# Kernel optimization log

Hardware: AMD Instinct MI355X
Metric: run time of the kernel (lower is better)

## Reference

```python
import jax, jax.numpy as jnp
import numpy as np

C, H, W = 3, 2048, 2048
N_ANN = 64
P = 512  # patch resolution
RESIZE_FRAC = 0.5  # deterministic midpoint of resize_range=(0.25, 0.75)
MIN_SIZE = 10


def setup_inputs() -> dict:
    key = jax.random.key(0)
    k1, k2, k3, k4 = jax.random.split(key, 4)
    image = jax.random.normal(k1, (C, H, W), jnp.float32)
    patch = jax.random.uniform(k2, (C, P, P), jnp.float32)
    # build valid normalized xyxy boxes (x1<x2, y1<y2) inside the image
    centers = jax.random.uniform(k3, (N_ANN, 2), minval=0.2, maxval=0.8)
    sizes = jax.random.uniform(k4, (N_ANN, 2), minval=0.10, maxval=0.30)
    xy1 = jnp.clip(centers - sizes / 2, 0.0, 1.0)
    xy2 = jnp.clip(centers + sizes / 2, 0.0, 1.0)
    annotations = jnp.concatenate([xy1, xy2], axis=1).astype(jnp.float32)  # [N,4] xyxy
    return {"image": image, "annotations": annotations, "patch": patch}


def reference(image, annotations, patch):
    """MODE_CENTER_BBOX forward: for each bbox, bilinearly resize the patch to
    wh x wh (wh = min(bbox_w, bbox_h) * RESIZE_FRAC, >= MIN_SIZE), then paste it
    centered in the bbox (clamped to the image). embed_patch's mask arithmetic
    (image_mask*image + patch_mask*patch) is exactly a region overwrite."""
    c, h, w = image.shape
    # normalized_annotations=True: scale by [W, H, W, H] then floor to long
    ann = np.asarray(annotations * jnp.array([w, h, w, h], jnp.float32)).astype(np.int64)
    img = image
    for x1, y1, x2, y2 in ann:
        bw, bh = int(x2 - x1), int(y2 - y1)
        wh = max(int(min(bw, bh) * RESIZE_FRAC), MIN_SIZE)
        rp = jax.image.resize(patch, (c, wh, wh), method="bilinear")
        x = int(x1) + bw // 2 - wh // 2
        y = int(y1) + bh // 2 - wh // 2
        y = max(min(h - wh, y), 0)
        x = max(min(w - wh, x), 0)
        img = img.at[:, y:y + wh, x:x + wh].set(rp)
    return img
```

## Files before the change

kernel.cpp:

```cpp
#include <hip/hip_runtime.h>

#define CCH 3
#define HH 2048
#define WW 2048
#define NANN 64
#define PSZ 512
#define HWIMG (HH * WW)
#define PP (PSZ * PSZ)
#define WHMAX 308
#define OYB 4
#define CHS ((size_t)PSZ * WHMAX)

__global__ void prep_kernel(const float* __restrict__ ann, int* __restrict__ meta) {
    int a = threadIdx.x;
    if (a >= NANN) return;
    float x1f = ann[a * 4 + 0] * (float)WW;
    float y1f = ann[a * 4 + 1] * (float)HH;
    float x2f = ann[a * 4 + 2] * (float)WW;
    float y2f = ann[a * 4 + 3] * (float)HH;
    int x1 = (int)x1f, y1 = (int)y1f, x2 = (int)x2f, y2 = (int)y2f;
    int bw = x2 - x1, bh = y2 - y1;
    int mn = bw < bh ? bw : bh;
    int wh = mn / 2;
    if (wh < 10) wh = 10;
    int x = x1 + bw / 2 - wh / 2;
    int y = y1 + bh / 2 - wh / 2;
    y = min(HH - wh, y); y = max(y, 0);
    x = min(WW - wh, x); x = max(x, 0);
    meta[a * 4 + 0] = x;
    meta[a * 4 + 1] = y;
    meta[a * 4 + 2] = wh;
    meta[a * 4 + 3] = 0;
}

__global__ __launch_bounds__(256) void resize_y4_kernel(
    const float* __restrict__ patch, const int* __restrict__ meta,
    float* __restrict__ tmp)
{
    const int a   = blockIdx.y;
    const int oy0 = blockIdx.x * OYB;
    const int wh  = meta[a * 4 + 2];
    if (oy0 >= wh) return;

    const int xx = threadIdx.x * 2;
    const float inv = 512.0f / (float)wh;
    const float rs  = (float)wh / 512.0f;

    float syf[OYB];
#pragma unroll
    for (int i = 0; i < OYB; ++i)
        syf[i] = ((float)(oy0 + i) + 0.5f) * inv - 0.5f;

    const int ylast = min(oy0 + OYB - 1, wh - 1);
    const float syfL = ((float)ylast + 0.5f) * inv - 0.5f;
    const int ylo = max(0,       (int)ceilf(syf[0] - inv));
    const int yhi = min(PSZ - 1, (int)floorf(syfL + inv));

    float2 ac[OYB][3];
    float dy[OYB];
#pragma unroll
    for (int i = 0; i < OYB; ++i) {
        dy[i] = 0.f;
#pragma unroll
        for (int c = 0; c < 3; ++c) { ac[i][c].x = 0.f; ac[i][c].y = 0.f; }
    }

    const float* p = patch + xx;
#pragma unroll 2
    for (int yy = ylo; yy <= yhi; ++yy) {
        const float* row = p + yy * PSZ;
        float2 v0 = *(const float2*)(row);
        float2 v1 = *(const float2*)(row + PP);
        float2 v2 = *(const float2*)(row + 2 * PP);
#pragma unroll
        for (int i = 0; i < OYB; ++i) {
            float w = fmaxf(0.f, 1.f - fabsf(syf[i] - (float)yy) * rs);
            dy[i] += w;
            ac[i][0].x = fmaf(w, v0.x, ac[i][0].x);
            ac[i][0].y = fmaf(w, v0.y, ac[i][0].y);
            ac[i][1].x = fmaf(w, v1.x, ac[i][1].x);
            ac[i][1].y = fmaf(w, v1.y, ac[i][1].y);
            ac[i][2].x = fmaf(w, v2.x, ac[i][2].x);
            ac[i][2].y = fmaf(w, v2.y, ac[i][2].y);
        }
    }

#pragma unroll
    for (int i = 0; i < OYB; ++i) {
        int oy = oy0 + i;
        if (oy < wh) {
            float s = 1.0f / dy[i];
            float* t = tmp + ((size_t)(a * 3) * WHMAX + oy) * PSZ + xx;
            float2 o0 = { ac[i][0].x * s, ac[i][0].y * s };
            float2 o1 = { ac[i][1].x * s, ac[i][1].y * s };
            float2 o2 = { ac[i][2].x * s, ac[i][2].y * s };
            *(float2*)(t)           = o0;
            *(float2*)(t + CHS)     = o1;
            *(float2*)(t + 2 * CHS) = o2;
        }
    }
}

__global__ __launch_bounds__(256) void composite_kernel(
    const float* __restrict__ img, const float* __restrict__ tmp,
    const int* __restrict__ meta, float* __restrict__ out)
{
    __shared__ int sax[NANN], say[NANN], sawh[NANN];
    __shared__ unsigned long long smask;

    const int tid = threadIdx.x;
    const int bx = blockIdx.x * 64;
    const int by = blockIdx.y * 4;

    if (tid < NANN) {
        int x = meta[tid * 4 + 0];
        int y = meta[tid * 4 + 1];
        int wh = meta[tid * 4 + 2];
        sax[tid] = x; say[tid] = y; sawh[tid] = wh;
        bool ov = (x < bx + 64) && (x + wh > bx) && (y < by + 4) && (y + wh > by);
        unsigned long long m = __ballot(ov);
        if (tid == 0) smask = m;
    }
    __syncthreads();

    const int px = bx + (tid & 63);
    const int py = by + (tid >> 6);
    const int idx = py * WW + px;

    unsigned long long m = smask;
    int hit = -1;
    while (m) {
        int a = 63 - __clzll(m);
        if (px >= sax[a] && px < sax[a] + sawh[a] &&
            py >= say[a] && py < say[a] + sawh[a]) { hit = a; break; }
        m &= ~(1ull << a);
    }

    if (hit < 0) {
        out[idx]             = img[idx];
        out[idx + HWIMG]     = img[idx + HWIMG];
        out[idx + 2 * HWIMG] = img[idx + 2 * HWIMG];
        return;
    }

    const int wh = sawh[hit];
    const int jx = px - sax[hit];
    const int jy = py - say[hit];

    const float inv = 512.0f / (float)wh;
    const float rs  = (float)wh / 512.0f;
    const float sxf = ((float)jx + 0.5f) * inv - 0.5f;
    const int xlo = max(0,       (int)ceilf(sxf - inv));
    const int xhi = min(PSZ - 1, (int)floorf(sxf + inv));

    int kstart = xlo & ~3;
    if (kstart > 496) kstart = 496;

    const float* tb = tmp + ((size_t)(hit * 3) * WHMAX + jy) * PSZ;

    if (xhi - kstart <= 15) {
        float r0[16], r1[16], r2[16];
#pragma unroll
        for (int u = 0; u < 4; ++u) {
            float4 qa = *(const float4*)(tb + kstart + 4 * u);
            float4 qb = *(const float4*)(tb + CHS + kstart + 4 * u);
            float4 qc = *(const float4*)(tb + 2 * CHS + kstart + 4 * u);
            r0[4 * u + 0] = qa.x; r0[4 * u + 1] = qa.y; r0[4 * u + 2] = qa.z; r0[4 * u + 3] = qa.w;
            r1[4 * u + 0] = qb.x; r1[4 * u + 1] = qb.y; r1[4 * u + 2] = qb.z; r1[4 * u + 3] = qb.w;
            r2[4 * u + 0] = qc.x; r2[4 * u + 1] = qc.y; r2[4 * u + 2] = qc.z; r2[4 * u + 3] = qc.w;
        }
        float dx = 0.f, a0 = 0.f, a1 = 0.f, a2 = 0.f;
#pragma unroll
        for (int j = 0; j < 16; ++j) {
            int pos = kstart + j;
            float w = (pos <= xhi) ? fmaxf(0.f, 1.f - fabsf(sxf - (float)pos) * rs) : 0.f;
            dx += w;
            a0 = fmaf(w, r0[j], a0);
            a1 = fmaf(w, r1[j], a1);
            a2 = fmaf(w, r2[j], a2);
        }
        const float s = 1.0f / dx;
        out[idx]             = a0 * s;
        out[idx + HWIMG]     = a1 * s;
        out[idx + 2 * HWIMG] = a2 * s;
    } else {
        float dx = 0.f;
        for (int x = xlo; x <= xhi; ++x)
            dx += fmaxf(0.f, 1.f - fabsf(sxf - (float)x) * rs);
        float a0 = 0.f, a1 = 0.f, a2 = 0.f;
        for (int x = xlo; x <= xhi; ++x) {
            float w = fmaxf(0.f, 1.f - fabsf(sxf - (float)x) * rs);
            a0 = fmaf(w, tb[x],           a0);
            a1 = fmaf(w, tb[x + CHS],     a1);
            a2 = fmaf(w, tb[x + 2 * CHS], a2);
        }
        const float s = 1.0f / dx;
        out[idx]             = a0 * s;
        out[idx + HWIMG]     = a1 * s;
        out[idx + 2 * HWIMG] = a2 * s;
    }
}

extern "C" void kernel_launch(void* const* d_in, const int* in_sizes, int n_in,
                              void* d_out, int out_size, void* d_ws, size_t ws_size,
                              hipStream_t stream) {
    const float* img   = (const float*)d_in[0];
    const float* ann   = (const float*)d_in[1];
    const float* patch = (const float*)d_in[2];
    float* out = (float*)d_out;

    int*   meta = (int*)d_ws;
    float* tmp  = (float*)((char*)d_ws + 4096);

    hipLaunchKernelGGL(prep_kernel, dim3(1), dim3(64), 0, stream, ann, meta);
    hipLaunchKernelGGL(resize_y4_kernel, dim3((WHMAX + OYB - 1) / OYB, NANN), dim3(256),
                       0, stream, patch, meta, tmp);
    hipLaunchKernelGGL(composite_kernel, dim3(WW / 64, HH / 4), dim3(256), 0, stream,
                       img, tmp, meta, out);
}
```

Before: 61.01 us.

## Replace full-image composite with memcpy plus per-annotation paste kernel

The per-pixel composite kernel, which scanned annotation masks over the whole image, is replaced. The image is now copied to the output with a device-to-device memcpy, and a paste kernel then walks only each annotation's patch region. A pixel is skipped when a later annotation covers it, which keeps last-writer-wins semantics without any ordering between blocks. The aim is to stop running overlap searches over pixels that no box touches. The cost is that overlapped pixels get an O(N) later-box check, and the output region is written twice (copy, then paste).

```diff
diff --git a/kernel.cpp b/kernel.cpp
--- a/kernel.cpp
+++ b/kernel.cpp
@@ -101,51 +101,37 @@
     }
 }
 
-__global__ __launch_bounds__(256) void composite_kernel(
-    const float* __restrict__ img, const float* __restrict__ tmp,
-    const int* __restrict__ meta, float* __restrict__ out)
+__global__ __launch_bounds__(256) void paste_kernel(
+    const float* __restrict__ tmp, const int* __restrict__ meta,
+    float* __restrict__ out)
 {
     __shared__ int sax[NANN], say[NANN], sawh[NANN];
-    __shared__ unsigned long long smask;
+
+    const int a  = blockIdx.z;
+    const int wh = meta[a * 4 + 2];
+    const int jx0 = blockIdx.x * 64;
+    const int jy0 = blockIdx.y * 4;
+    if (jx0 >= wh || jy0 >= wh) return;
 
     const int tid = threadIdx.x;
-    const int bx = blockIdx.x * 64;
-    const int by = blockIdx.y * 4;
-
     if (tid < NANN) {
-        int x = meta[tid * 4 + 0];
-        int y = meta[tid * 4 + 1];
-        int wh = meta[tid * 4 + 2];
-        sax[tid] = x; say[tid] = y; sawh[tid] = wh;
-        bool ov = (x < bx + 64) && (x + wh > bx) && (y < by + 4) && (y + wh > by);
-        unsigned long long m = __ballot(ov);
-        if (tid == 0) smask = m;
+        sax[tid]  = meta[tid * 4 + 0];
+        say[tid]  = meta[tid * 4 + 1];
+        sawh[tid] = meta[tid * 4 + 2];
     }
     __syncthreads();
 
-    const int px = bx + (tid & 63);
-    const int py = by + (tid >> 6);
-    const int idx = py * WW + px;
-
-    unsigned long long m = smask;
-    int hit = -1;
-    while (m) {
-        int a = 63 - __clzll(m);
-        if (px >= sax[a] && px < sax[a] + sawh[a] &&
-            py >= say[a] && py < say[a] + sawh[a]) { hit = a; break; }
-        m &= ~(1ull << a);
-    }
-
-    if (hit < 0) {
-        out[idx]             = img[idx];
-        out[idx + HWIMG]     = img[idx + HWIMG];
-        out[idx + 2 * HWIMG] = img[idx + 2 * HWIMG];
-        return;
-    }
-
-    const int wh = sawh[hit];
-    const int jx = px - sax[hit];
-    const int jy = py - say[hit];
+    const int jx = jx0 + (tid & 63);
+    const int jy = jy0 + (tid >> 6);
+    if (jx >= wh || jy >= wh) return;
+
+    const int px = sax[a] + jx;
+    const int py = say[a] + jy;
+
+    for (int b = a + 1; b < NANN; ++b) {
+        if (px >= sax[b] && px < sax[b] + sawh[b] &&
+            py >= say[b] && py < say[b] + sawh[b]) return;
+    }
 
     const float inv = 512.0f / (float)wh;
     const float rs  = (float)wh / 512.0f;
@@ -156,7 +142,8 @@
     int kstart = xlo & ~3;
     if (kstart > 496) kstart = 496;
 
-    const float* tb = tmp + ((size_t)(hit * 3) * WHMAX + jy) * PSZ;
+    const float* tb = tmp + ((size_t)(a * 3) * WHMAX + jy) * PSZ;
+    const int idx = py * WW + px;
 
     if (xhi - kstart <= 15) {
         float r0[16], r1[16], r2[16];
@@ -215,6 +202,9 @@
     hipLaunchKernelGGL(prep_kernel, dim3(1), dim3(64), 0, stream, ann, meta);
     hipLaunchKernelGGL(resize_y4_kernel, dim3((WHMAX + OYB - 1) / OYB, NANN), dim3(256),
                        0, stream, patch, meta, tmp);
-    hipLaunchKernelGGL(composite_kernel, dim3(WW / 64, HH / 4), dim3(256), 0, stream,
-                       img, tmp, meta, out);
-}
+    hipMemcpyAsync(out, img, (size_t)out_size * sizeof(float),
+                   hipMemcpyDeviceToDevice, stream);
+    hipLaunchKernelGGL(paste_kernel,
+                       dim3((WHMAX + 63) / 64, (WHMAX + 3) / 4, NANN), dim3(256),
+                       0, stream, tmp, meta, out);
+}
```

After: 94.66 us. 55.2% more time.

## Widen composite tiles, add float4 fast path, swizzle block order, add 8-tap path

Applied to the files above, without the earlier changes.

Each composite block now covers a 256x4 tile instead of 64x4, with each thread handling four pixels. Tiles that no box overlaps take a float4 copy fast path. Block IDs are permuted with a multiplicative hash, which should spread patch-covered tiles evenly across compute units. The horizontal resample gains an 8-tap specialisation for small patches, loading only two float4s per channel. The costs are fewer blocks and more per-thread work in overlapped tiles, which may reduce latency hiding.

```diff
diff --git a/kernel.cpp b/kernel.cpp
--- a/kernel.cpp
+++ b/kernel.cpp
@@ -10,6 +10,9 @@
 #define WHMAX 308
 #define OYB 4
 #define CHS ((size_t)PSZ * WHMAX)
+#define GX (WW / 256)
+#define GY (HH / 4)
+#define NTILE (GX * GY)
 
 __global__ void prep_kernel(const float* __restrict__ ann, int* __restrict__ meta) {
     int a = threadIdx.x;
@@ -101,6 +104,81 @@
     }
 }
 
+__device__ __forceinline__ void resample_px(
+    const float* __restrict__ tmp, int a, int wh, int jx, int jy,
+    float* __restrict__ out, int idx)
+{
+    const float inv = 512.0f / (float)wh;
+    const float rs  = (float)wh / 512.0f;
+    const float sxf = ((float)jx + 0.5f) * inv - 0.5f;
+    const int xlo = max(0,       (int)ceilf(sxf - inv));
+    const int xhi = min(PSZ - 1, (int)floorf(sxf + inv));
+
+    const float* tb = tmp + ((size_t)(a * 3) * WHMAX + jy) * PSZ;
+    float dx = 0.f, a0 = 0.f, a1 = 0.f, a2 = 0.f;
+
+    const int ka = xlo & ~3;
+    const int k8 = min(ka, 504);
+
+    if (xhi - k8 <= 7) {
+        float wgt[8];
+#pragma unroll
+        for (int j = 0; j < 8; ++j) {
+            int pos = k8 + j;
+            float w = (pos <= xhi) ? fmaxf(0.f, 1.f - fabsf(sxf - (float)pos) * rs) : 0.f;
+            wgt[j] = w; dx += w;
+        }
+#pragma unroll
+        for (int u = 0; u < 2; ++u) {
+            float4 qa = *(const float4*)(tb + k8 + 4 * u);
+            float4 qb = *(const float4*)(tb + CHS + k8 + 4 * u);
+            float4 qc = *(const float4*)(tb + 2 * CHS + k8 + 4 * u);
+            a0 = fmaf(wgt[4*u+0], qa.x, a0); a0 = fmaf(wgt[4*u+1], qa.y, a0);
+            a0 = fmaf(wgt[4*u+2], qa.z, a0); a0 = fmaf(wgt[4*u+3], qa.w, a0);
+            a1 = fmaf(wgt[4*u+0], qb.x, a1); a1 = fmaf(wgt[4*u+1], qb.y, a1);
+            a1 = fmaf(wgt[4*u+2], qb.z, a1); a1 = fmaf(wgt[4*u+3], qb.w, a1);
+            a2 = fmaf(wgt[4*u+0], qc.x, a2); a2 = fmaf(wgt[4*u+1], qc.y, a2);
+            a2 = fmaf(wgt[4*u+2], qc.z, a2); a2 = fmaf(wgt[4*u+3], qc.w, a2);
+        }
+    } else {
+        const int k16 = min(ka, 496);
+        if (xhi - k16 <= 15) {
+            float wgt[16];
+#pragma unroll
+            for (int j = 0; j < 16; ++j) {
+                int pos = k16 + j;
+                float w = (pos <= xhi) ? fmaxf(0.f, 1.f - fabsf(sxf - (float)pos) * rs) : 0.f;
+                wgt[j] = w; dx += w;
+            }
+#pragma unroll
+            for (int u = 0; u < 4; ++u) {
+                float4 qa = *(const float4*)(tb + k16 + 4 * u);
+                float4 qb = *(const float4*)(tb + CHS + k16 + 4 * u);
+                float4 qc = *(const float4*)(tb + 2 * CHS + k16 + 4 * u);
+                a0 = fmaf(wgt[4*u+0], qa.x, a0); a0 = fmaf(wgt[4*u+1], qa.y, a0);
+                a0 = fmaf(wgt[4*u+2], qa.z, a0); a0 = fmaf(wgt[4*u+3], qa.w, a0);
+                a1 = fmaf(wgt[4*u+0], qb.x, a1); a1 = fmaf(wgt[4*u+1], qb.y, a1);
+                a1 = fmaf(wgt[4*u+2], qb.z, a1); a1 = fmaf(wgt[4*u+3], qb.w, a1);
+                a2 = fmaf(wgt[4*u+0], qc.x, a2); a2 = fmaf(wgt[4*u+1], qc.y, a2);
+                a2 = fmaf(wgt[4*u+2], qc.z, a2); a2 = fmaf(wgt[4*u+3], qc.w, a2);
+            }
+        } else {
+            for (int x = xlo; x <= xhi; ++x)
+                dx += fmaxf(0.f, 1.f - fabsf(sxf - (float)x) * rs);
+            for (int x = xlo; x <= xhi; ++x) {
+                float w = fmaxf(0.f, 1.f - fabsf(sxf - (float)x) * rs);
+                a0 = fmaf(w, tb[x],           a0);
+                a1 = fmaf(w, tb[x + CHS],     a1);
+                a2 = fmaf(w, tb[x + 2 * CHS], a2);
+            }
+        }
+    }
+    const float s = 1.0f / dx;
+    out[idx]             = a0 * s;
+    out[idx + HWIMG]     = a1 * s;
+    out[idx + 2 * HWIMG] = a2 * s;
+}
+
 __global__ __launch_bounds__(256) void composite_kernel(
     const float* __restrict__ img, const float* __restrict__ tmp,
     const int* __restrict__ meta, float* __restrict__ out)
@@ -109,95 +187,57 @@
     __shared__ unsigned long long smask;
 
     const int tid = threadIdx.x;
-    const int bx = blockIdx.x * 64;
-    const int by = blockIdx.y * 4;
+    const int lid = blockIdx.y * GX + blockIdx.x;
+    const int sid = (lid * 1543) & (NTILE - 1);
+    const int bx = (sid & (GX - 1)) * 256;
+    const int by = (sid / GX) * 4;
 
     if (tid < NANN) {
         int x = meta[tid * 4 + 0];
         int y = meta[tid * 4 + 1];
         int wh = meta[tid * 4 + 2];
         sax[tid] = x; say[tid] = y; sawh[tid] = wh;
-        bool ov = (x < bx + 64) && (x + wh > bx) && (y < by + 4) && (y + wh > by);
-        unsigned long long m = __ballot(ov);
-        if (tid == 0) smask = m;
+        bool ov = (x < bx + 256) && (x + wh > bx) && (y < by + 4) && (y + wh > by);
+        unsigned long long mm = __ballot(ov);
+        if (tid == 0) smask = mm;
     }
     __syncthreads();
 
-    const int px = bx + (tid & 63);
+    const unsigned long long tmask = smask;
+
+    if (tmask == 0) {
+        const int x0  = bx + (tid & 63) * 4;
+        const int py  = by + (tid >> 6);
+        const int idx = py * WW + x0;
+        *(float4*)(out + idx)             = *(const float4*)(img + idx);
+        *(float4*)(out + idx + HWIMG)     = *(const float4*)(img + idx + HWIMG);
+        *(float4*)(out + idx + 2 * HWIMG) = *(const float4*)(img + idx + 2 * HWIMG);
+        return;
+    }
+
+    const int lx = tid & 63;
     const int py = by + (tid >> 6);
-    const int idx = py * WW + px;
-
-    unsigned long long m = smask;
-    int hit = -1;
-    while (m) {
-        int a = 63 - __clzll(m);
-        if (px >= sax[a] && px < sax[a] + sawh[a] &&
-            py >= say[a] && py < say[a] + sawh[a]) { hit = a; break; }
-        m &= ~(1ull << a);
-    }
-
-    if (hit < 0) {
-        out[idx]             = img[idx];
-        out[idx + HWIMG]     = img[idx + HWIMG];
-        out[idx + 2 * HWIMG] = img[idx + 2 * HWIMG];
-        return;
-    }
-
-    const int wh = sawh[hit];
-    const int jx = px - sax[hit];
-    const int jy = py - say[hit];
-
-    const float inv = 512.0f / (float)wh;
-    const float rs  = (float)wh / 512.0f;
-    const float sxf = ((float)jx + 0.5f) * inv - 0.5f;
-    const int xlo = max(0,       (int)ceilf(sxf - inv));
-    const int xhi = min(PSZ - 1, (int)floorf(sxf + inv));
-
-    int kstart = xlo & ~3;
-    if (kstart > 496) kstart = 496;
-
-    const float* tb = tmp + ((size_t)(hit * 3) * WHMAX + jy) * PSZ;
-
-    if (xhi - kstart <= 15) {
-        float r0[16], r1[16], r2[16];
-#pragma unroll
-        for (int u = 0; u < 4; ++u) {
-            float4 qa = *(const float4*)(tb + kstart + 4 * u);
-            float4 qb = *(const float4*)(tb + CHS + kstart + 4 * u);
-            float4 qc = *(const float4*)(tb + 2 * CHS + kstart + 4 * u);
-            r0[4 * u + 0] = qa.x; r0[4 * u + 1] = qa.y; r0[4 * u + 2] = qa.z; r0[4 * u + 3] = qa.w;
-            r1[4 * u + 0] = qb.x; r1[4 * u + 1] = qb.y; r1[4 * u + 2] = qb.z; r1[4 * u + 3] = qb.w;
-            r2[4 * u + 0] = qc.x; r2[4 * u + 1] = qc.y; r2[4 * u + 2] = qc.z; r2[4 * u + 3] = qc.w;
-        }
-        float dx = 0.f, a0 = 0.f, a1 = 0.f, a2 = 0.f;
-#pragma unroll
-        for (int j = 0; j < 16; ++j) {
-            int pos = kstart + j;
-            float w = (pos <= xhi) ? fmaxf(0.f, 1.f - fabsf(sxf - (float)pos) * rs) : 0.f;
-            dx += w;
-            a0 = fmaf(w, r0[j], a0);
-            a1 = fmaf(w, r1[j], a1);
-            a2 = fmaf(w, r2[j], a2);
-        }
-        const float s = 1.0f / dx;
-        out[idx]             = a0 * s;
-        out[idx + HWIMG]     = a1 * s;
-        out[idx + 2 * HWIMG] = a2 * s;
-    } else {
-        float dx = 0.f;
-        for (int x = xlo; x <= xhi; ++x)
-            dx += fmaxf(0.f, 1.f - fabsf(sxf - (float)x) * rs);
-        float a0 = 0.f, a1 = 0.f, a2 = 0.f;
-        for (int x = xlo; x <= xhi; ++x) {
-            float w = fmaxf(0.f, 1.f - fabsf(sxf - (float)x) * rs);
-            a0 = fmaf(w, tb[x],           a0);
-            a1 = fmaf(w, tb[x + CHS],     a1);
-            a2 = fmaf(w, tb[x + 2 * CHS], a2);
-        }
-        const float s = 1.0f / dx;
-        out[idx]             = a0 * s;
-        out[idx + HWIMG]     = a1 * s;
-        out[idx + 2 * HWIMG] = a2 * s;
+#pragma unroll
+    for (int it = 0; it < 4; ++it) {
+        const int px  = bx + it * 64 + lx;
+        const int idx = py * WW + px;
+
+        unsigned long long m = tmask;
+        int hit = -1;
+        while (m) {
+            int a = 63 - __clzll(m);
+            if (px >= sax[a] && px < sax[a] + sawh[a] &&
+                py >= say[a] && py < say[a] + sawh[a]) { hit = a; break; }
+            m &= ~(1ull << a);
+        }
+
+        if (hit < 0) {
+            out[idx]             = img[idx];
+            out[idx + HWIMG]     = img[idx + HWIMG];
+            out[idx + 2 * HWIMG] = img[idx + 2 * HWIMG];
+        } else {
+            resample_px(tmp, hit, sawh[hit], px - sax[hit], py - say[hit], out, idx);
+        }
     }
 }
 
@@ -215,6 +255,6 @@
     hipLaunchKernelGGL(prep_kernel, dim3(1), dim3(64), 0, stream, ann, meta);
     hipLaunchKernelGGL(resize_y4_kernel, dim3((WHMAX + OYB - 1) / OYB, NANN), dim3(256),
                        0, stream, patch, meta, tmp);
-    hipLaunchKernelGGL(composite_kernel, dim3(WW / 64, HH / 4), dim3(256), 0, stream,
+    hipLaunchKernelGGL(composite_kernel, dim3(GX, GY), dim3(256), 0, stream,
                        img, tmp, meta, out);
 }
```

After: 66.85 us. 1.1x slower.
